# Kernel tuning notes

Measured on AMD Instinct MI355X. Metric: run time of the kernel, lower is better.

## Reference

```python
import jax, jax.numpy as jnp
import numpy as np

B, S, D, H = 2, 2048, 512, 8
HID = 512
DH = HID // H  # 64


def setup_inputs() -> dict:
    key = jax.random.key(0)
    ks = jax.random.split(key, 11)
    sc = 0.02
    return {
        "q": jax.random.normal(ks[0], (B, S, D), jnp.float32),
        "k": jax.random.normal(ks[1], (B, S, D), jnp.float32),
        "v": jax.random.normal(ks[2], (B, S, D), jnp.float32),
        "Wq": jax.random.normal(ks[3], (D, HID), jnp.float32) * sc,
        "bq": jnp.zeros((HID,), jnp.float32),
        "Wk": jax.random.normal(ks[4], (D, HID), jnp.float32) * sc,
        "bk": jnp.zeros((HID,), jnp.float32),
        "Wv": jax.random.normal(ks[5], (D, HID), jnp.float32) * sc,
        "bv": jnp.zeros((HID,), jnp.float32),
        "Wo": jax.random.normal(ks[6], (HID, D), jnp.float32) * sc,
        "bo": jnp.zeros((D,), jnp.float32),
    }


def reference(q, k, v, Wq, bq, Wk, bk, Wv, bv, Wo, bo):
    # Linear projections: [B,S,D] -> [B,S,HID]
    qp = q @ Wq + bq
    kp = k @ Wk + bk
    vp = v @ Wv + bv
    # Faithful to torch .view(B, -1, S, head_dim): raw reshape, NOT a
    # [B,S,H,d] transpose. Head i reads a contiguous block of the buffer.
    qh = qp.reshape(B, H, S, DH)
    kh = kp.reshape(B, H, S, DH)
    vh = vp.reshape(B, H, S, DH)
    # scores [B,H,S,S]; NOTE: original divides by sqrt(d) AFTER softmax.
    scores = jnp.einsum("bhsd,bhtd->bhst", qh, kh)
    attn = jax.nn.softmax(scores, axis=-1) / np.sqrt(DH).astype(np.float32)
    ctx = jnp.einsum("bhst,bhtd->bhsd", attn, vh)
    # torch.cat over heads along last dim -> [B,S,H*d] with head blocks
    concat = jnp.transpose(ctx, (0, 2, 1, 3)).reshape(B, S, HID)
    return concat @ Wo + bo
```

## Files before the change

### kernel.cpp

```cpp
#include <hip/hip_runtime.h>
#include <hip/hip_bf16.h>

typedef __bf16 bf16_t;
typedef __bf16 bf16x8 __attribute__((ext_vector_type(8)));
typedef __bf16 bf16x4 __attribute__((ext_vector_type(4)));
typedef short short4v __attribute__((ext_vector_type(4)));
typedef float f32x4 __attribute__((ext_vector_type(4)));

static_assert(sizeof(bf16x8) == 16, "bf16x8 must be 16B");

#define BB 2
#define SS 2048
#define DD 512
#define HH 8
#define DH 64

__global__ void cast_qkv(const float* __restrict__ q, const float* __restrict__ k,
                         const float* __restrict__ v, bf16_t* __restrict__ dst, int n) {
  const float* src = (blockIdx.z == 0) ? q : (blockIdx.z == 1) ? k : v;
  bf16_t* out = dst + (size_t)blockIdx.z * n;
  int i = (blockIdx.x * 256 + threadIdx.x) * 8;
  if (i >= n) return;
  const float4* s4 = (const float4*)(src + i);
  float4 a = s4[0], b = s4[1];
  bf16x8 o;
  o[0] = (bf16_t)a.x; o[1] = (bf16_t)a.y; o[2] = (bf16_t)a.z; o[3] = (bf16_t)a.w;
  o[4] = (bf16_t)b.x; o[5] = (bf16_t)b.y; o[6] = (bf16_t)b.z; o[7] = (bf16_t)b.w;
  *(bf16x8*)(out + i) = o;
}

__global__ void transpose_w(const float* __restrict__ w0, const float* __restrict__ w1,
                            const float* __restrict__ w2, const float* __restrict__ w3,
                            bf16_t* __restrict__ wt) {
  __shared__ float tile[32][33];
  const float* W = (blockIdx.z == 0) ? w0 : (blockIdx.z == 1) ? w1 : (blockIdx.z == 2) ? w2 : w3;
  bf16_t* out = wt + (size_t)blockIdx.z * 512 * 512;
  int tx = threadIdx.x, ty = threadIdx.y;
  int nb = blockIdx.x * 32, kb = blockIdx.y * 32;
#pragma unroll
  for (int i = 0; i < 4; i++)
    tile[ty + i * 8][tx] = W[(size_t)(kb + ty + i * 8) * 512 + nb + tx];
  __syncthreads();
#pragma unroll
  for (int i = 0; i < 4; i++)
    out[(size_t)(nb + ty + i * 8) * 512 + kb + tx] = (bf16_t)tile[tx][ty + i * 8];
}

template <typename OutT>
__global__ __launch_bounds__(256) void gemm_bt(
    const bf16_t* __restrict__ Abase, const bf16_t* __restrict__ Btbase,
    const float* __restrict__ bias0, const float* __restrict__ bias1,
    const float* __restrict__ bias2, OutT* __restrict__ Cbase,
    int M, int N, int K, long Az, long Bz, long Cz) {
  const bf16_t* A  = Abase + (size_t)blockIdx.z * Az;
  const bf16_t* Bt = Btbase + (size_t)blockIdx.z * Bz;
  const float* bias = (blockIdx.z == 0) ? bias0 : (blockIdx.z == 1) ? bias1 : bias2;
  OutT* C = Cbase + (size_t)blockIdx.z * Cz;

  __shared__ bf16_t As[2][128 * 64];
  __shared__ bf16_t Bs[2][128 * 64];

  const int tid = threadIdx.x, w = tid >> 6, l = tid & 63;
  const int bm = blockIdx.y, bn = blockIdx.x;
  const int wm = (w >> 1) * 64, wn = (w & 1) * 64;
  const int lr = l & 15, lg = l >> 4;

  f32x4 acc[4][4] = {};

  auto stage = [&](int buf, int kt) {
#pragma unroll
    for (int j = 0; j < 4; j++) {
      int lin = (j * 4 + w) * 64 + l;
      int row = lin >> 3, cc = lin & 7;
      const bf16_t* g = A + (size_t)(bm * 128 + row) * K + kt * 64 + cc * 8;
      __builtin_amdgcn_global_load_lds(
          (const __attribute__((address_space(1))) void*)g,
          (__attribute__((address_space(3))) void*)(&As[buf][(j * 4 + w) * 512]), 16, 0, 0);
    }
#pragma unroll
    for (int j = 0; j < 4; j++) {
      int lin = (j * 4 + w) * 64 + l;
      int row = lin >> 3, cc = lin & 7;
      const bf16_t* g = Bt + (size_t)(bn * 128 + row) * K + kt * 64 + cc * 8;
      __builtin_amdgcn_global_load_lds(
          (const __attribute__((address_space(1))) void*)g,
          (__attribute__((address_space(3))) void*)(&Bs[buf][(j * 4 + w) * 512]), 16, 0, 0);
    }
  };

  stage(0, 0);
  const int KT = K >> 6;
  for (int kt = 0; kt < KT; kt++) {
    __syncthreads();
    if (kt + 1 < KT) stage((kt + 1) & 1, kt + 1);
    const bf16_t* as = As[kt & 1];
    const bf16_t* bs = Bs[kt & 1];
#pragma unroll
    for (int kc = 0; kc < 2; kc++) {
      bf16x8 a[4], b[4];
#pragma unroll
      for (int i = 0; i < 4; i++)
        a[i] = *(const bf16x8*)(as + (wm + i * 16 + lr) * 64 + kc * 32 + lg * 8);
#pragma unroll
      for (int i = 0; i < 4; i++)
        b[i] = *(const bf16x8*)(bs + (wn + i * 16 + lr) * 64 + kc * 32 + lg * 8);
#pragma unroll
      for (int i = 0; i < 4; i++)
#pragma unroll
        for (int j = 0; j < 4; j++)
          acc[i][j] = __builtin_amdgcn_mfma_f32_16x16x32_bf16(a[i], b[j], acc[i][j], 0, 0, 0);
    }
  }

  const int row0 = bm * 128 + wm, col0 = bn * 128 + wn;
#pragma unroll
  for (int j = 0; j < 4; j++) {
    int col = col0 + j * 16 + lr;
    float bv = bias[col];
#pragma unroll
    for (int i = 0; i < 4; i++) {
      int row = row0 + i * 16 + lg * 4;
#pragma unroll
      for (int r = 0; r < 4; r++) {
        float vv = acc[i][j][r] + bv;
        C[(size_t)(row + r) * N + col] = (OutT)vv;
      }
    }
  }
}

__global__ __launch_bounds__(256) void attn_flash(const bf16_t* __restrict__ qp,
                                                  const bf16_t* __restrict__ kp,
                                                  const bf16_t* __restrict__ vp,
                                                  float* __restrict__ Opart,
                                                  float* __restrict__ mlpart) {
  const int id = blockIdx.x;
  const int bh = (id & 7) | (((id >> 3) & 1) << 3);
  const int qt = (id >> 4) & 31;
  const int half = id >> 9;
  const int pidx = ((qt << 4) | bh) * 2 + half;

  const int tid = threadIdx.x, w = tid >> 6, l = tid & 63;
  const int lr = l & 15, lg = l >> 4;
  const size_t hb = (size_t)bh * (SS * DH);
  const bf16_t* Q = qp + hb;
  const bf16_t* Kh = kp + hb;
  const bf16_t* Vh = vp + hb;

  __shared__ bf16_t Ks[2][64][72];
  __shared__ bf16_t Vt[2][64][72];

  const int qr0 = qt * 64 + w * 16;

  bf16x8 aq[2];
#pragma unroll
  for (int kc = 0; kc < 2; kc++)
    aq[kc] = *(const bf16x8*)(Q + (size_t)(qr0 + lr) * DH + kc * 32 + lg * 8);

  f32x4 o[4] = {};
  float m_run = -1e30f, l_run = 0.f;

  const int c0 = tid, c1 = 256 + tid;
  const int kr0 = c0 >> 3, kq0 = c0 & 7;
  const int kr1 = c1 >> 3, kq1 = c1 & 7;
  const int vk0 = c0 & 63, vd0 = (c0 >> 6) & 7;
  const int vk1 = c1 & 63, vd1 = (c1 >> 6) & 7;

  bf16x8 kreg0, kreg1, vreg0, vreg1;
  auto load_g = [&](int it) {
    const size_t kv0 = (size_t)it * 64;
    kreg0 = *(const bf16x8*)(Kh + (kv0 + kr0) * DH + kq0 * 8);
    kreg1 = *(const bf16x8*)(Kh + (kv0 + kr1) * DH + kq1 * 8);
    vreg0 = *(const bf16x8*)(Vh + (kv0 + vk0) * DH + vd0 * 8);
    vreg1 = *(const bf16x8*)(Vh + (kv0 + vk1) * DH + vd1 * 8);
  };
  auto write_lds = [&](int buf) {
    *(bf16x8*)(&Ks[buf][kr0][kq0 * 8]) = kreg0;
    *(bf16x8*)(&Ks[buf][kr1][kq1 * 8]) = kreg1;
#pragma unroll
    for (int j = 0; j < 8; j++) Vt[buf][vd0 * 8 + j][vk0] = vreg0[j];
#pragma unroll
    for (int j = 0; j < 8; j++) Vt[buf][vd1 * 8 + j][vk1] = vreg1[j];
  };

  const int it0 = half * 16;
  load_g(it0);
  write_lds(0);

  for (int i = 0; i < 16; i++) {
    const int buf = i & 1;
    __syncthreads();
    if (i + 1 < 16) load_g(it0 + i + 1);

    f32x4 s[4] = {};
    __builtin_amdgcn_s_setprio(1);
#pragma unroll
    for (int kc = 0; kc < 2; kc++) {
#pragma unroll
      for (int n = 0; n < 4; n++) {
        bf16x8 bk = *(const bf16x8*)(&Ks[buf][n * 16 + lr][kc * 32 + lg * 8]);
        s[n] = __builtin_amdgcn_mfma_f32_16x16x32_bf16(bk, aq[kc], s[n], 0, 0, 0);
      }
    }
    __builtin_amdgcn_s_setprio(0);

    float pmax = -1e30f;
#pragma unroll
    for (int n = 0; n < 4; n++)
#pragma unroll
      for (int r = 0; r < 4; r++) pmax = fmaxf(pmax, s[n][r]);
    pmax = fmaxf(pmax, __shfl_xor(pmax, 16));
    pmax = fmaxf(pmax, __shfl_xor(pmax, 32));
    if (!__all(pmax <= m_run + 8.0f)) {
      float mnew = fmaxf(m_run, pmax);
      float scale = __expf(m_run - mnew);
      l_run *= scale;
#pragma unroll
      for (int n = 0; n < 4; n++)
#pragma unroll
        for (int r = 0; r < 4; r++) o[n][r] *= scale;
      m_run = mnew;
    }
    float rs = 0.f;
#pragma unroll
    for (int n = 0; n < 4; n++)
#pragma unroll
      for (int r = 0; r < 4; r++) {
        float e = __expf(s[n][r] - m_run);
        s[n][r] = e;
        rs += e;
      }
    rs += __shfl_xor(rs, 16);
    rs += __shfl_xor(rs, 32);
    l_run += rs;

    short4v pb[4];
#pragma unroll
    for (int n = 0; n < 4; n++) {
      bf16x4 t;
#pragma unroll
      for (int r = 0; r < 4; r++) t[r] = (bf16_t)s[n][r];
      pb[n] = __builtin_bit_cast(short4v, t);
    }
    __builtin_amdgcn_s_setprio(1);
#pragma unroll
    for (int n = 0; n < 4; n++) {
#pragma unroll
      for (int c2 = 0; c2 < 4; c2++) {
        bf16x4 bvh = *(const bf16x4*)(&Vt[buf][n * 16 + lr][c2 * 16 + lg * 4]);
        o[n] = __builtin_amdgcn_mfma_f32_16x16x16bf16_1k(
            __builtin_bit_cast(short4v, bvh), pb[c2], o[n], 0, 0, 0);
      }
    }
    __builtin_amdgcn_s_setprio(0);

    if (i + 1 < 16) write_lds(buf ^ 1);
  }

  float* ob = Opart + (size_t)pidx * 4096;
#pragma unroll
  for (int n = 0; n < 4; n++)
    *(f32x4*)(ob + ((w * 4 + n) * 64 + l) * 4) = o[n];
  if (lg == 0) {
    mlpart[(size_t)pidx * 128 + (w * 16 + lr) * 2 + 0] = m_run;
    mlpart[(size_t)pidx * 128 + (w * 16 + lr) * 2 + 1] = l_run;
  }
}

__global__ __launch_bounds__(256) void attn_combine(const float* __restrict__ Opart,
                                                    const float* __restrict__ mlpart,
                                                    bf16_t* __restrict__ ctx) {
  const int id = blockIdx.x;
  const int qt = id >> 4, bh = id & 15;
  const int t = threadIdx.x, w = t >> 6, l = t & 63;
  const int lr = l & 15, lg = l >> 4;
  const int p0 = id * 2, p1 = id * 2 + 1;
  const int q = w * 16 + lr;

  float m1 = mlpart[(size_t)p0 * 128 + q * 2 + 0];
  float l1 = mlpart[(size_t)p0 * 128 + q * 2 + 1];
  float m2 = mlpart[(size_t)p1 * 128 + q * 2 + 0];
  float l2 = mlpart[(size_t)p1 * 128 + q * 2 + 1];
  float m = fmaxf(m1, m2);
  float e1 = __expf(m1 - m), e2 = __expf(m2 - m);
  float denom = (l1 * e1 + l2 * e2) * 8.0f;
  float f1 = e1 / denom, f2 = e2 / denom;

  const int b = bh >> 3, h = bh & 7;
  const int trow = qt * 64 + q;
  size_t rowbase = ((size_t)b * SS + trow) * 512 + h * 64;

  const float* oa = Opart + (size_t)p0 * 4096;
  const float* obp = Opart + (size_t)p1 * 4096;
#pragma unroll
  for (int n = 0; n < 4; n++) {
    f32x4 a = *(const f32x4*)(oa + ((w * 4 + n) * 64 + l) * 4);
    f32x4 b2 = *(const f32x4*)(obp + ((w * 4 + n) * 64 + l) * 4);
    bf16x4 ov;
#pragma unroll
    for (int r = 0; r < 4; r++) ov[r] = (bf16_t)(a[r] * f1 + b2[r] * f2);
    *(bf16x4*)(&ctx[rowbase + n * 16 + lg * 4]) = ov;
  }
}

extern "C" void kernel_launch(void* const* d_in, const int* in_sizes, int n_in,
                              void* d_out, int out_size, void* d_ws, size_t ws_size,
                              hipStream_t stream) {
  const float* q  = (const float*)d_in[0];
  const float* k  = (const float*)d_in[1];
  const float* v  = (const float*)d_in[2];
  const float* Wq = (const float*)d_in[3];
  const float* bq = (const float*)d_in[4];
  const float* Wk = (const float*)d_in[5];
  const float* bk = (const float*)d_in[6];
  const float* Wv = (const float*)d_in[7];
  const float* bv = (const float*)d_in[8];
  const float* Wo = (const float*)d_in[9];
  const float* bo = (const float*)d_in[10];

  const size_t NQKV = (size_t)4096 * 512;
  const size_t NW = (size_t)512 * 512;

  bf16_t* ws   = (bf16_t*)d_ws;
  bf16_t* wt   = ws;
  bf16_t* proj = wt + 4 * NW;
  bf16_t* ctx  = proj + 3 * NQKV;
  bf16_t* qkvb = ctx + NQKV;
  float* Opart  = (float*)qkvb;
  float* mlpart = Opart + (size_t)1024 * 4096;

  cast_qkv<<<dim3(1024, 1, 3), 256, 0, stream>>>(q, k, v, qkvb, (int)NQKV);
  transpose_w<<<dim3(16, 16, 4), dim3(32, 8), 0, stream>>>(Wq, Wk, Wv, Wo, wt);
  gemm_bt<bf16_t><<<dim3(4, 32, 3), 256, 0, stream>>>(
      qkvb, wt, bq, bk, bv, proj, 4096, 512, 512, (long)NQKV, (long)NW, (long)NQKV);
  attn_flash<<<1024, 256, 0, stream>>>(proj, proj + NQKV, proj + 2 * NQKV, Opart, mlpart);
  attn_combine<<<512, 256, 0, stream>>>(Opart, mlpart, ctx);
  gemm_bt<float><<<dim3(4, 32, 1), 256, 0, stream>>>(
      ctx, wt + 3 * NW, bo, bo, bo, (float*)d_out, 4096, 512, 512, 0, 0, 0);
}
```

Before: 91.83 us.

## Fuse split-KV combine into attention via atomic flags, swizzle LDS, merge prep kernels

The cast and weight-transpose kernels are merged into one prep launch. The separate attn_combine kernel is removed. Instead, the second of the two split-KV blocks to finish, detected with an atomic counter per tile, reads its partner's partial output and writes the normalized bf16 context directly. LDS tiles for K and V^T switch from padded arrays to XOR-swizzled layouts to avoid bank conflicts. This saves launches and a round trip of one partial buffer, at the cost of a memset, threadfences and an atomic.

```diff
diff --git a/kernel.cpp b/kernel.cpp
--- a/kernel.cpp
+++ b/kernel.cpp
@@ -15,35 +15,39 @@
 #define HH 8
 #define DH 64
 
-__global__ void cast_qkv(const float* __restrict__ q, const float* __restrict__ k,
-                         const float* __restrict__ v, bf16_t* __restrict__ dst, int n) {
-  const float* src = (blockIdx.z == 0) ? q : (blockIdx.z == 1) ? k : v;
-  bf16_t* out = dst + (size_t)blockIdx.z * n;
-  int i = (blockIdx.x * 256 + threadIdx.x) * 8;
-  if (i >= n) return;
-  const float4* s4 = (const float4*)(src + i);
-  float4 a = s4[0], b = s4[1];
-  bf16x8 o;
-  o[0] = (bf16_t)a.x; o[1] = (bf16_t)a.y; o[2] = (bf16_t)a.z; o[3] = (bf16_t)a.w;
-  o[4] = (bf16_t)b.x; o[5] = (bf16_t)b.y; o[6] = (bf16_t)b.z; o[7] = (bf16_t)b.w;
-  *(bf16x8*)(out + i) = o;
-}
-
-__global__ void transpose_w(const float* __restrict__ w0, const float* __restrict__ w1,
-                            const float* __restrict__ w2, const float* __restrict__ w3,
-                            bf16_t* __restrict__ wt) {
-  __shared__ float tile[32][33];
-  const float* W = (blockIdx.z == 0) ? w0 : (blockIdx.z == 1) ? w1 : (blockIdx.z == 2) ? w2 : w3;
-  bf16_t* out = wt + (size_t)blockIdx.z * 512 * 512;
-  int tx = threadIdx.x, ty = threadIdx.y;
-  int nb = blockIdx.x * 32, kb = blockIdx.y * 32;
-#pragma unroll
-  for (int i = 0; i < 4; i++)
-    tile[ty + i * 8][tx] = W[(size_t)(kb + ty + i * 8) * 512 + nb + tx];
-  __syncthreads();
-#pragma unroll
-  for (int i = 0; i < 4; i++)
-    out[(size_t)(nb + ty + i * 8) * 512 + kb + tx] = (bf16_t)tile[tx][ty + i * 8];
+__global__ void prep(const float* __restrict__ q, const float* __restrict__ k,
+                     const float* __restrict__ v, const float* __restrict__ w0,
+                     const float* __restrict__ w1, const float* __restrict__ w2,
+                     const float* __restrict__ w3, bf16_t* __restrict__ qkvb,
+                     bf16_t* __restrict__ wt, int n) {
+  const int tid = threadIdx.x;
+  if (blockIdx.z < 3) {
+    const float* src = (blockIdx.z == 0) ? q : (blockIdx.z == 1) ? k : v;
+    bf16_t* out = qkvb + (size_t)blockIdx.z * n;
+    int i = (blockIdx.x * 256 + tid) * 8;
+    if (i >= n) return;
+    const float4* s4 = (const float4*)(src + i);
+    float4 a = s4[0], b = s4[1];
+    bf16x8 o;
+    o[0] = (bf16_t)a.x; o[1] = (bf16_t)a.y; o[2] = (bf16_t)a.z; o[3] = (bf16_t)a.w;
+    o[4] = (bf16_t)b.x; o[5] = (bf16_t)b.y; o[6] = (bf16_t)b.z; o[7] = (bf16_t)b.w;
+    *(bf16x8*)(out + i) = o;
+  } else {
+    __shared__ float tile[32][33];
+    const int x = blockIdx.x;
+    const int wsel = x >> 8;
+    const int nb = ((x >> 4) & 15) * 32, kb = (x & 15) * 32;
+    const int tx = tid & 31, ty = tid >> 5;
+    const float* W = (wsel == 0) ? w0 : (wsel == 1) ? w1 : (wsel == 2) ? w2 : w3;
+    bf16_t* out = wt + (size_t)wsel * 512 * 512;
+#pragma unroll
+    for (int i = 0; i < 4; i++)
+      tile[ty + i * 8][tx] = W[(size_t)(kb + ty + i * 8) * 512 + nb + tx];
+    __syncthreads();
+#pragma unroll
+    for (int i = 0; i < 4; i++)
+      out[(size_t)(nb + ty + i * 8) * 512 + kb + tx] = (bf16_t)tile[tx][ty + i * 8];
+  }
 }
 
 template <typename OutT>
@@ -133,12 +137,15 @@
                                                   const bf16_t* __restrict__ kp,
                                                   const bf16_t* __restrict__ vp,
                                                   float* __restrict__ Opart,
-                                                  float* __restrict__ mlpart) {
+                                                  float* __restrict__ mlpart,
+                                                  int* __restrict__ flags,
+                                                  bf16_t* __restrict__ ctx) {
   const int id = blockIdx.x;
   const int bh = (id & 7) | (((id >> 3) & 1) << 3);
   const int qt = (id >> 4) & 31;
   const int half = id >> 9;
-  const int pidx = ((qt << 4) | bh) * 2 + half;
+  const int gid = (qt << 4) | bh;
+  const int pidx = gid * 2 + half;
 
   const int tid = threadIdx.x, w = tid >> 6, l = tid & 63;
   const int lr = l & 15, lg = l >> 4;
@@ -147,8 +154,7 @@
   const bf16_t* Kh = kp + hb;
   const bf16_t* Vh = vp + hb;
 
-  __shared__ bf16_t Ks[2][64][72];
-  __shared__ bf16_t Vt[2][64][72];
+  __shared__ __align__(16) unsigned char smem[32768];
 
   const int qr0 = qt * 64 + w * 16;
 
@@ -175,12 +181,20 @@
     vreg1 = *(const bf16x8*)(Vh + (kv0 + vk1) * DH + vd1 * 8);
   };
   auto write_lds = [&](int buf) {
-    *(bf16x8*)(&Ks[buf][kr0][kq0 * 8]) = kreg0;
-    *(bf16x8*)(&Ks[buf][kr1][kq1 * 8]) = kreg1;
-#pragma unroll
-    for (int j = 0; j < 8; j++) Vt[buf][vd0 * 8 + j][vk0] = vreg0[j];
-#pragma unroll
-    for (int j = 0; j < 8; j++) Vt[buf][vd1 * 8 + j][vk1] = vreg1[j];
+    unsigned char* ks = smem + buf * 8192;
+    unsigned char* vt = smem + 16384 + buf * 8192;
+    *(bf16x8*)(ks + kr0 * 128 + ((kq0 * 16) ^ ((kr0 & 7) << 4))) = kreg0;
+    *(bf16x8*)(ks + kr1 * 128 + ((kq1 * 16) ^ ((kr1 & 7) << 4))) = kreg1;
+#pragma unroll
+    for (int j = 0; j < 8; j++) {
+      int d0 = vd0 * 8 + j;
+      *(bf16_t*)(vt + d0 * 128 + ((vk0 * 2) ^ ((d0 & 7) << 4))) = vreg0[j];
+    }
+#pragma unroll
+    for (int j = 0; j < 8; j++) {
+      int d1 = vd1 * 8 + j;
+      *(bf16_t*)(vt + d1 * 128 + ((vk1 * 2) ^ ((d1 & 7) << 4))) = vreg1[j];
+    }
   };
 
   const int it0 = half * 16;
@@ -192,13 +206,17 @@
     __syncthreads();
     if (i + 1 < 16) load_g(it0 + i + 1);
 
+    const unsigned char* ks = smem + buf * 8192;
+    const unsigned char* vt = smem + 16384 + buf * 8192;
+
     f32x4 s[4] = {};
     __builtin_amdgcn_s_setprio(1);
 #pragma unroll
     for (int kc = 0; kc < 2; kc++) {
 #pragma unroll
       for (int n = 0; n < 4; n++) {
-        bf16x8 bk = *(const bf16x8*)(&Ks[buf][n * 16 + lr][kc * 32 + lg * 8]);
+        bf16x8 bk = *(const bf16x8*)(ks + (n * 16 + lr) * 128 +
+                                     ((kc * 64 + lg * 16) ^ ((lr & 7) << 4)));
         s[n] = __builtin_amdgcn_mfma_f32_16x16x32_bf16(bk, aq[kc], s[n], 0, 0, 0);
       }
     }
@@ -247,7 +265,8 @@
     for (int n = 0; n < 4; n++) {
 #pragma unroll
       for (int c2 = 0; c2 < 4; c2++) {
-        bf16x4 bvh = *(const bf16x4*)(&Vt[buf][n * 16 + lr][c2 * 16 + lg * 4]);
+        bf16x4 bvh = *(const bf16x4*)(vt + (n * 16 + lr) * 128 +
+                                      ((c2 * 32 + lg * 8) ^ ((lr & 7) << 4)));
         o[n] = __builtin_amdgcn_mfma_f32_16x16x16bf16_1k(
             __builtin_bit_cast(short4v, bvh), pb[c2], o[n], 0, 0, 0);
       }
@@ -265,40 +284,40 @@
     mlpart[(size_t)pidx * 128 + (w * 16 + lr) * 2 + 0] = m_run;
     mlpart[(size_t)pidx * 128 + (w * 16 + lr) * 2 + 1] = l_run;
   }
-}
-
-__global__ __launch_bounds__(256) void attn_combine(const float* __restrict__ Opart,
-                                                    const float* __restrict__ mlpart,
-                                                    bf16_t* __restrict__ ctx) {
-  const int id = blockIdx.x;
-  const int qt = id >> 4, bh = id & 15;
-  const int t = threadIdx.x, w = t >> 6, l = t & 63;
-  const int lr = l & 15, lg = l >> 4;
-  const int p0 = id * 2, p1 = id * 2 + 1;
-  const int q = w * 16 + lr;
-
-  float m1 = mlpart[(size_t)p0 * 128 + q * 2 + 0];
-  float l1 = mlpart[(size_t)p0 * 128 + q * 2 + 1];
-  float m2 = mlpart[(size_t)p1 * 128 + q * 2 + 0];
-  float l2 = mlpart[(size_t)p1 * 128 + q * 2 + 1];
-  float m = fmaxf(m1, m2);
-  float e1 = __expf(m1 - m), e2 = __expf(m2 - m);
-  float denom = (l1 * e1 + l2 * e2) * 8.0f;
-  float f1 = e1 / denom, f2 = e2 / denom;
-
+
+  __threadfence();
+  __syncthreads();
+  volatile int* shflag = (volatile int*)smem;
+  if (tid == 0) shflag[0] = atomicAdd(&flags[gid], 1);
+  __syncthreads();
+  if (shflag[0] == 0) return;
+  __threadfence();
+
+  const int partner = gid * 2 + (half ^ 1);
+  float mO = mlpart[(size_t)partner * 128 + (w * 16 + lr) * 2 + 0];
+  float lO = mlpart[(size_t)partner * 128 + (w * 16 + lr) * 2 + 1];
+  float m = fmaxf(m_run, mO);
+  float fM = __expf(m_run - m), fO = __expf(mO - m);
+  float lA = (half == 0) ? l_run * fM : lO * fO;
+  float lB = (half == 0) ? lO * fO : l_run * fM;
+  float inv = 1.0f / ((lA + lB) * 8.0f);
+  float gM = (half == 0) ? fM : fO;
+  (void)gM;
+
+  const float* obp = Opart + (size_t)partner * 4096;
   const int b = bh >> 3, h = bh & 7;
-  const int trow = qt * 64 + q;
-  size_t rowbase = ((size_t)b * SS + trow) * 512 + h * 64;
-
-  const float* oa = Opart + (size_t)p0 * 4096;
-  const float* obp = Opart + (size_t)p1 * 4096;
+  const int t = qr0 + lr;
+  size_t rowbase = ((size_t)b * SS + t) * 512 + h * 64;
 #pragma unroll
   for (int n = 0; n < 4; n++) {
-    f32x4 a = *(const f32x4*)(oa + ((w * 4 + n) * 64 + l) * 4);
-    f32x4 b2 = *(const f32x4*)(obp + ((w * 4 + n) * 64 + l) * 4);
+    f32x4 po = *(const f32x4*)(obp + ((w * 4 + n) * 64 + l) * 4);
     bf16x4 ov;
 #pragma unroll
-    for (int r = 0; r < 4; r++) ov[r] = (bf16_t)(a[r] * f1 + b2[r] * f2);
+    for (int r = 0; r < 4; r++) {
+      float a = (half == 0) ? o[n][r] * fM : po[r] * fO;
+      float bt = (half == 0) ? po[r] * fO : o[n][r] * fM;
+      ov[r] = (bf16_t)((a + bt) * inv);
+    }
     *(bf16x4*)(&ctx[rowbase + n * 16 + lg * 4]) = ov;
   }
 }
@@ -328,13 +347,14 @@
   bf16_t* qkvb = ctx + NQKV;
   float* Opart  = (float*)qkvb;
   float* mlpart = Opart + (size_t)1024 * 4096;
-
-  cast_qkv<<<dim3(1024, 1, 3), 256, 0, stream>>>(q, k, v, qkvb, (int)NQKV);
-  transpose_w<<<dim3(16, 16, 4), dim3(32, 8), 0, stream>>>(Wq, Wk, Wv, Wo, wt);
+  int*   flags  = (int*)(mlpart + (size_t)1024 * 128);
+
+  hipMemsetAsync(flags, 0, 512 * sizeof(int), stream);
+  prep<<<dim3(1024, 1, 4), 256, 0, stream>>>(q, k, v, Wq, Wk, Wv, Wo, qkvb, wt, (int)NQKV);
   gemm_bt<bf16_t><<<dim3(4, 32, 3), 256, 0, stream>>>(
       qkvb, wt, bq, bk, bv, proj, 4096, 512, 512, (long)NQKV, (long)NW, (long)NQKV);
-  attn_flash<<<1024, 256, 0, stream>>>(proj, proj + NQKV, proj + 2 * NQKV, Opart, mlpart);
-  attn_combine<<<512, 256, 0, stream>>>(Opart, mlpart, ctx);
+  attn_flash<<<1024, 256, 0, stream>>>(proj, proj + NQKV, proj + 2 * NQKV,
+                                       Opart, mlpart, flags, ctx);
   gemm_bt<float><<<dim3(4, 32, 1), 256, 0, stream>>>(
       ctx, wt + 3 * NW, bo, bo, bo, (float*)d_out, 4096, 512, 512, 0, 0, 0);
 }
```

Result: slower. 241.5 us (+163.0%).

## Stage K via direct global-to-LDS loads with XOR swizzle; merge prep kernels

Applied to the files above, without the earlier changes.

The attention kernel now copies K tiles straight from global memory into LDS with global_load_lds, skipping the register round trip. K and the transposed V tiles use unpadded 128-byte rows with an XOR swizzle to avoid bank conflicts, and the V store pattern gives each lane one key column. The cast and weight-transpose kernels are merged into one launch to save a kernel launch. The risk is that the direct-to-LDS addressing and swizzle must line up with the MFMA read pattern, and the merged prep kernel gives some blocks nothing to do.

```diff
diff --git a/kernel.cpp b/kernel.cpp
--- a/kernel.cpp
+++ b/kernel.cpp
@@ -15,35 +15,39 @@
 #define HH 8
 #define DH 64
 
-__global__ void cast_qkv(const float* __restrict__ q, const float* __restrict__ k,
-                         const float* __restrict__ v, bf16_t* __restrict__ dst, int n) {
-  const float* src = (blockIdx.z == 0) ? q : (blockIdx.z == 1) ? k : v;
-  bf16_t* out = dst + (size_t)blockIdx.z * n;
-  int i = (blockIdx.x * 256 + threadIdx.x) * 8;
-  if (i >= n) return;
-  const float4* s4 = (const float4*)(src + i);
-  float4 a = s4[0], b = s4[1];
-  bf16x8 o;
-  o[0] = (bf16_t)a.x; o[1] = (bf16_t)a.y; o[2] = (bf16_t)a.z; o[3] = (bf16_t)a.w;
-  o[4] = (bf16_t)b.x; o[5] = (bf16_t)b.y; o[6] = (bf16_t)b.z; o[7] = (bf16_t)b.w;
-  *(bf16x8*)(out + i) = o;
-}
-
-__global__ void transpose_w(const float* __restrict__ w0, const float* __restrict__ w1,
-                            const float* __restrict__ w2, const float* __restrict__ w3,
-                            bf16_t* __restrict__ wt) {
-  __shared__ float tile[32][33];
-  const float* W = (blockIdx.z == 0) ? w0 : (blockIdx.z == 1) ? w1 : (blockIdx.z == 2) ? w2 : w3;
-  bf16_t* out = wt + (size_t)blockIdx.z * 512 * 512;
-  int tx = threadIdx.x, ty = threadIdx.y;
-  int nb = blockIdx.x * 32, kb = blockIdx.y * 32;
-#pragma unroll
-  for (int i = 0; i < 4; i++)
-    tile[ty + i * 8][tx] = W[(size_t)(kb + ty + i * 8) * 512 + nb + tx];
-  __syncthreads();
-#pragma unroll
-  for (int i = 0; i < 4; i++)
-    out[(size_t)(nb + ty + i * 8) * 512 + kb + tx] = (bf16_t)tile[tx][ty + i * 8];
+__global__ void prep(const float* __restrict__ q, const float* __restrict__ k,
+                     const float* __restrict__ v, const float* __restrict__ w0,
+                     const float* __restrict__ w1, const float* __restrict__ w2,
+                     const float* __restrict__ w3, bf16_t* __restrict__ qkvb,
+                     bf16_t* __restrict__ wt, int n) {
+  const int tid = threadIdx.x;
+  if (blockIdx.z < 3) {
+    const float* src = (blockIdx.z == 0) ? q : (blockIdx.z == 1) ? k : v;
+    bf16_t* out = qkvb + (size_t)blockIdx.z * n;
+    int i = (blockIdx.x * 256 + tid) * 8;
+    if (i >= n) return;
+    const float4* s4 = (const float4*)(src + i);
+    float4 a = s4[0], b = s4[1];
+    bf16x8 o;
+    o[0] = (bf16_t)a.x; o[1] = (bf16_t)a.y; o[2] = (bf16_t)a.z; o[3] = (bf16_t)a.w;
+    o[4] = (bf16_t)b.x; o[5] = (bf16_t)b.y; o[6] = (bf16_t)b.z; o[7] = (bf16_t)b.w;
+    *(bf16x8*)(out + i) = o;
+  } else {
+    __shared__ float tile[32][33];
+    const int x = blockIdx.x;
+    const int wsel = x >> 8;
+    const int nb = ((x >> 4) & 15) * 32, kb = (x & 15) * 32;
+    const int tx = tid & 31, ty = tid >> 5;
+    const float* W = (wsel == 0) ? w0 : (wsel == 1) ? w1 : (wsel == 2) ? w2 : w3;
+    bf16_t* out = wt + (size_t)wsel * 512 * 512;
+#pragma unroll
+    for (int i = 0; i < 4; i++)
+      tile[ty + i * 8][tx] = W[(size_t)(kb + ty + i * 8) * 512 + nb + tx];
+    __syncthreads();
+#pragma unroll
+    for (int i = 0; i < 4; i++)
+      out[(size_t)(nb + ty + i * 8) * 512 + kb + tx] = (bf16_t)tile[tx][ty + i * 8];
+  }
 }
 
 template <typename OutT>
@@ -138,7 +142,7 @@
   const int bh = (id & 7) | (((id >> 3) & 1) << 3);
   const int qt = (id >> 4) & 31;
   const int half = id >> 9;
-  const int pidx = ((qt << 4) | bh) * 2 + half;
+  const int pidx = (((qt << 4) | bh) << 1) + half;
 
   const int tid = threadIdx.x, w = tid >> 6, l = tid & 63;
   const int lr = l & 15, lg = l >> 4;
@@ -147,8 +151,8 @@
   const bf16_t* Kh = kp + hb;
   const bf16_t* Vh = vp + hb;
 
-  __shared__ bf16_t Ks[2][64][72];
-  __shared__ bf16_t Vt[2][64][72];
+  __shared__ __align__(16) bf16_t KsL[2][4096];
+  __shared__ __align__(16) bf16_t VtL[2][4096];
 
   const int qr0 = qt * 64 + w * 16;
 
@@ -160,45 +164,62 @@
   f32x4 o[4] = {};
   float m_run = -1e30f, l_run = 0.f;
 
-  const int c0 = tid, c1 = 256 + tid;
-  const int kr0 = c0 >> 3, kq0 = c0 & 7;
-  const int kr1 = c1 >> 3, kq1 = c1 & 7;
-  const int vk0 = c0 & 63, vd0 = (c0 >> 6) & 7;
-  const int vk1 = c1 & 63, vd1 = (c1 >> 6) & 7;
-
-  bf16x8 kreg0, kreg1, vreg0, vreg1;
-  auto load_g = [&](int it) {
+  const int krow = (w << 3) + (l >> 3);
+  const int kcol = ((l & 7) ^ (l >> 3)) << 3;
+  const bf16_t* ks_it = Kh + (size_t)(half * 16) * 4096 + krow * 64 + kcol;
+
+  auto stage_k = [&](int buf, const bf16_t* ks) {
+    char* kb = (char*)&KsL[buf][0];
+    __builtin_amdgcn_global_load_lds((const __attribute__((address_space(1))) void*)ks,
+        (__attribute__((address_space(3))) void*)(kb + (w << 10)), 16, 0, 0);
+    __builtin_amdgcn_global_load_lds((const __attribute__((address_space(1))) void*)(ks + 2048),
+        (__attribute__((address_space(3))) void*)(kb + 4096 + (w << 10)), 16, 0, 0);
+  };
+
+  const int vk0 = l, vd0 = w;
+  const int vd1 = 4 + w;
+  bf16x8 vreg0, vreg1;
+  auto load_v = [&](int it) {
     const size_t kv0 = (size_t)it * 64;
-    kreg0 = *(const bf16x8*)(Kh + (kv0 + kr0) * DH + kq0 * 8);
-    kreg1 = *(const bf16x8*)(Kh + (kv0 + kr1) * DH + kq1 * 8);
     vreg0 = *(const bf16x8*)(Vh + (kv0 + vk0) * DH + vd0 * 8);
-    vreg1 = *(const bf16x8*)(Vh + (kv0 + vk1) * DH + vd1 * 8);
+    vreg1 = *(const bf16x8*)(Vh + (kv0 + vk0) * DH + vd1 * 8);
   };
-  auto write_lds = [&](int buf) {
-    *(bf16x8*)(&Ks[buf][kr0][kq0 * 8]) = kreg0;
-    *(bf16x8*)(&Ks[buf][kr1][kq1 * 8]) = kreg1;
-#pragma unroll
-    for (int j = 0; j < 8; j++) Vt[buf][vd0 * 8 + j][vk0] = vreg0[j];
-#pragma unroll
-    for (int j = 0; j < 8; j++) Vt[buf][vd1 * 8 + j][vk1] = vreg1[j];
+  auto write_v = [&](int buf) {
+    char* vt = (char*)&VtL[buf][0];
+#pragma unroll
+    for (int j = 0; j < 8; j++) {
+      int d0 = vd0 * 8 + j;
+      *(bf16_t*)(vt + d0 * 128 + ((vk0 * 2) ^ (j << 4))) = vreg0[j];
+    }
+#pragma unroll
+    for (int j = 0; j < 8; j++) {
+      int d1 = vd1 * 8 + j;
+      *(bf16_t*)(vt + d1 * 128 + ((vk0 * 2) ^ (j << 4))) = vreg1[j];
+    }
   };
 
-  const int it0 = half * 16;
-  load_g(it0);
-  write_lds(0);
+  stage_k(0, ks_it);
+  load_v(half * 16);
+  write_v(0);
 
   for (int i = 0; i < 16; i++) {
     const int buf = i & 1;
     __syncthreads();
-    if (i + 1 < 16) load_g(it0 + i + 1);
-
+    if (i + 1 < 16) {
+      ks_it += 4096;
+      stage_k(buf ^ 1, ks_it);
+      load_v(half * 16 + i + 1);
+    }
+
+    const char* ksb = (const char*)&KsL[buf][0];
     f32x4 s[4] = {};
     __builtin_amdgcn_s_setprio(1);
 #pragma unroll
     for (int kc = 0; kc < 2; kc++) {
 #pragma unroll
       for (int n = 0; n < 4; n++) {
-        bf16x8 bk = *(const bf16x8*)(&Ks[buf][n * 16 + lr][kc * 32 + lg * 8]);
+        bf16x8 bk = *(const bf16x8*)(ksb + (n * 16 + lr) * 128 +
+                                     ((kc * 64 + lg * 16) ^ ((lr & 7) << 4)));
         s[n] = __builtin_amdgcn_mfma_f32_16x16x32_bf16(bk, aq[kc], s[n], 0, 0, 0);
       }
     }
@@ -236,25 +257,27 @@
 
     short4v pb[4];
 #pragma unroll
+    for (int c2 = 0; c2 < 4; c2++) {
+      bf16x4 t;
+#pragma unroll
+      for (int r = 0; r < 4; r++) t[r] = (bf16_t)s[c2][r];
+      pb[c2] = __builtin_bit_cast(short4v, t);
+    }
+    const char* vtb = (const char*)&VtL[buf][0];
+    __builtin_amdgcn_s_setprio(1);
+#pragma unroll
     for (int n = 0; n < 4; n++) {
-      bf16x4 t;
-#pragma unroll
-      for (int r = 0; r < 4; r++) t[r] = (bf16_t)s[n][r];
-      pb[n] = __builtin_bit_cast(short4v, t);
-    }
-    __builtin_amdgcn_s_setprio(1);
-#pragma unroll
-    for (int n = 0; n < 4; n++) {
 #pragma unroll
       for (int c2 = 0; c2 < 4; c2++) {
-        bf16x4 bvh = *(const bf16x4*)(&Vt[buf][n * 16 + lr][c2 * 16 + lg * 4]);
+        bf16x4 bvh = *(const bf16x4*)(vtb + (n * 16 + lr) * 128 +
+                                      ((c2 * 32 + lg * 8) ^ ((lr & 7) << 4)));
         o[n] = __builtin_amdgcn_mfma_f32_16x16x16bf16_1k(
             __builtin_bit_cast(short4v, bvh), pb[c2], o[n], 0, 0, 0);
       }
     }
     __builtin_amdgcn_s_setprio(0);
 
-    if (i + 1 < 16) write_lds(buf ^ 1);
+    if (i + 1 < 16) write_v(buf ^ 1);
   }
 
   float* ob = Opart + (size_t)pidx * 4096;
@@ -329,8 +352,7 @@
   float* Opart  = (float*)qkvb;
   float* mlpart = Opart + (size_t)1024 * 4096;
 
-  cast_qkv<<<dim3(1024, 1, 3), 256, 0, stream>>>(q, k, v, qkvb, (int)NQKV);
-  transpose_w<<<dim3(16, 16, 4), dim3(32, 8), 0, stream>>>(Wq, Wk, Wv, Wo, wt);
+  prep<<<dim3(1024, 1, 4), 256, 0, stream>>>(q, k, v, Wq, Wk, Wv, Wo, qkvb, wt, (int)NQKV);
   gemm_bt<bf16_t><<<dim3(4, 32, 3), 256, 0, stream>>>(
       qkvb, wt, bq, bk, bv, proj, 4096, 512, 512, (long)NQKV, (long)NW, (long)NQKV);
   attn_flash<<<1024, 256, 0, stream>>>(proj, proj + NQKV, proj + 2 * NQKV, Opart, mlpart);
```

Measured after the change: 90.47 us. No clear change (-1.5%).
